# Kernel tuning notes

Hardware: AMD Instinct MI355X
Metric: run time of the kernel (lower is better)

The kernel has to match this reference:

```python
import jax, jax.numpy as jnp
import numpy as np

L = 12        # depth
DIM = 768     # model dim
HEADS = 12
DHEAD = 64
INNER = HEADS * DHEAD   # 768
MLP = 3072
P = 16        # patch size
IMG = 384
C = 3
B = 16
NCLS = 1000
NPATCH = (IMG // P) ** 2   # 576
N = NPATCH + 1             # 577 (cls token)
PATCH_DIM = C * P * P      # 768
SCALE = DIM ** (-0.5)      # NOTE: original scales by dim, not dim_head


def setup_inputs() -> dict:
    key = jax.random.key(0)
    ks = jax.random.split(key, 21)
    rn = lambda k, shape, s=0.02: jax.random.normal(k, shape, dtype=jnp.float32) * s
    return {
        "img": jax.random.normal(ks[0], (B, C, IMG, IMG), dtype=jnp.float32),
        "patch_w": rn(ks[1], (PATCH_DIM, DIM)),
        "patch_b": rn(ks[2], (DIM,)),
        "pos_emb": rn(ks[3], (1, N, DIM), 1.0),
        "cls_tok": rn(ks[4], (1, 1, DIM), 1.0),
        "ln1_w": jnp.ones((L, DIM), jnp.float32),
        "ln1_b": jnp.zeros((L, DIM), jnp.float32),
        "qkv_w": rn(ks[5], (L, DIM, 3 * INNER)),
        "out_w": rn(ks[6], (L, INNER, DIM)),
        "out_b": rn(ks[7], (L, DIM)),
        "ln2_w": jnp.ones((L, DIM), jnp.float32),
        "ln2_b": jnp.zeros((L, DIM), jnp.float32),
        "ff1_w": rn(ks[8], (L, DIM, MLP)),
        "ff1_b": rn(ks[9], (L, MLP)),
        "ff2_w": rn(ks[10], (L, MLP, DIM)),
        "ff2_b": rn(ks[11], (L, DIM)),
        "head_ln_w": jnp.ones((DIM,), jnp.float32),
        "head_ln_b": jnp.zeros((DIM,), jnp.float32),
        "head_w": rn(ks[12], (DIM, NCLS)),
        "head_b": rn(ks[13], (NCLS,)),
    }


def layer_norm(x, w, b, eps=1e-5):
    mu = jnp.mean(x, axis=-1, keepdims=True)
    var = jnp.mean(jnp.square(x - mu), axis=-1, keepdims=True)
    return (x - mu) * jax.lax.rsqrt(var + eps) * w + b


def _vit_forward(img, patch_w, patch_b, pos_emb, cls_tok,
                 ln1_w, ln1_b, qkv_w, out_w, out_b,
                 ln2_w, ln2_b, ff1_w, ff1_b, ff2_w, ff2_b,
                 head_ln_w, head_ln_b, head_w, head_b):
    b = img.shape[0]
    g = IMG // P
    # rearrange 'b c (h p1) (w p2) -> b (h w) (p1 p2 c)'
    x = img.reshape(b, C, g, P, g, P).transpose(0, 2, 4, 3, 5, 1).reshape(b, NPATCH, PATCH_DIM)
    x = x @ patch_w + patch_b                           # [b, 576, dim]
    cls = jnp.broadcast_to(cls_tok, (b, 1, DIM))
    x = jnp.concatenate([cls, x], axis=1) + pos_emb[:, :N]   # [b, 577, dim]

    def block(x, p):
        l1w, l1b, qkvw, ow, ob, l2w, l2b, f1w, f1b, f2w, f2b = p
        # attention (pre-norm, residual inside Attention.forward)
        h = layer_norm(x, l1w, l1b)
        qkv = h @ qkvw                                  # [b, n, 3*inner]
        q, k, v = jnp.split(qkv, 3, axis=-1)
        to_heads = lambda t: t.reshape(b, N, HEADS, DHEAD).transpose(0, 2, 1, 3)
        q, k, v = to_heads(q), to_heads(k), to_heads(v)  # [b, h, n, d]
        dots = jnp.einsum('bhid,bhjd->bhij', q, k) * SCALE
        attn = jax.nn.softmax(dots, axis=-1)
        o = jnp.einsum('bhij,bhjd->bhid', attn, v)
        o = o.transpose(0, 2, 1, 3).reshape(b, N, INNER)
        x = x + (o @ ow + ob)
        # feedforward (pre-norm, residual)
        h2 = layer_norm(x, l2w, l2b)
        h2 = jax.nn.gelu(h2 @ f1w + f1b, approximate=False)
        x = x + (h2 @ f2w + f2b)
        return x, None

    x, _ = jax.lax.scan(block, x,
                        (ln1_w, ln1_b, qkv_w, out_w, out_b,
                         ln2_w, ln2_b, ff1_w, ff1_b, ff2_w, ff2_b))
    cls_out = x[:, 0]                                   # [b, dim]
    return layer_norm(cls_out, head_ln_w, head_ln_b) @ head_w + head_b


def reference(img, patch_w, patch_b, pos_emb, cls_tok,
              ln1_w, ln1_b, qkv_w, out_w, out_b,
              ln2_w, ln2_b, ff1_w, ff1_b, ff2_w, ff2_b,
              head_ln_w, head_ln_b, head_w, head_b):
    return _vit_forward(img, patch_w, patch_b, pos_emb, cls_tok,
                        ln1_w, ln1_b, qkv_w, out_w, out_b,
                        ln2_w, ln2_b, ff1_w, ff1_b, ff2_w, ff2_b,
                        head_ln_w, head_ln_b, head_w, head_b)
```

## Files before the change

### kernel.cpp

```cpp
#include <hip/hip_runtime.h>
#include <cstdint>


typedef __attribute__((ext_vector_type(8))) short bf16x8;
typedef __attribute__((ext_vector_type(4))) float f32x4;

#define NTOK 577

__device__ __forceinline__ ushort f2bf(float f) {
  union { float f; unsigned int u; } x; x.f = f;
  unsigned int r = x.u + 0x7fffu + ((x.u >> 16) & 1u);
  return (ushort)(r >> 16);
}

__device__ __forceinline__ void gload_lds16(const ushort* g, ushort* l) {
  __builtin_amdgcn_global_load_lds(
      (const __attribute__((address_space(1))) unsigned int*)g,
      (__attribute__((address_space(3))) unsigned int*)l, 16, 0, 0);
}

#define VMCNT4 asm volatile("s_waitcnt vmcnt(4)" ::: "memory")
#define VMCNT2 asm volatile("s_waitcnt vmcnt(2)" ::: "memory")
#define VMCNT0 asm volatile("s_waitcnt vmcnt(0)" ::: "memory")
#define LGKM0  asm volatile("s_waitcnt lgkmcnt(0)" ::: "memory")
#define SCHED0 __builtin_amdgcn_sched_barrier(0)
#define BARRIER __builtin_amdgcn_s_barrier()

__device__ __forceinline__ int gsw(int row) {
  return (row & 7) + 2 * ((row >> 4) & 3);
}

__global__ __launch_bounds__(256) void convt_kernel(const float* __restrict__ W,
                                                    ushort* __restrict__ Wt,
                                                    int K, int N) {
  __shared__ float t[32][33];
  const int kb = blockIdx.x * 32, nb = blockIdx.y * 32;
  const int tx = threadIdx.x & 31, ty = threadIdx.x >> 5;
#pragma unroll
  for (int i = 0; i < 32; i += 8)
    t[ty + i][tx] = W[(size_t)(kb + ty + i) * N + (nb + tx)];
  __syncthreads();
#pragma unroll
  for (int i = 0; i < 32; i += 8)
    Wt[(size_t)(nb + ty + i) * K + (kb + tx)] = f2bf(t[tx][ty + i]);
}

__global__ __launch_bounds__(256) void im2col_kernel(const float* __restrict__ img,
                                                     ushort* __restrict__ Ap) {
  const int idx = blockIdx.x * 256 + threadIdx.x;
  const int j = idx % 768;
  const int m = idx / 768;
  const int c = j % 3;
  const int q = j / 3;
  const int px = q & 15, py = q >> 4;
  const int b = m / 576, p = m % 576;
  const int gy = p / 24, gx = p % 24;
  const float v = img[((size_t)(b * 3 + c) * 384 + (gy * 16 + py)) * 384 + (gx * 16 + px)];
  Ap[idx] = f2bf(v);
}

__global__ void clspos_kernel(const float* __restrict__ cls_tok,
                              const float* __restrict__ pos,
                              float* __restrict__ x) {
  const int i = blockIdx.x * 256 + threadIdx.x;
  const int b = i / 768, d = i % 768;
  x[(size_t)b * NTOK * 768 + d] = cls_tok[d] + pos[d];
}

__global__ __launch_bounds__(64) void ln_kernel(const float* __restrict__ x,
                                                const float* __restrict__ w,
                                                const float* __restrict__ bb,
                                                ushort* __restrict__ out) {
  const int row = blockIdx.x, lane = threadIdx.x;
  const float4* xr = reinterpret_cast<const float4*>(x + (size_t)row * 768);
  const float4 v0 = xr[lane], v1 = xr[lane + 64], v2 = xr[lane + 128];
  float vals[12] = {v0.x, v0.y, v0.z, v0.w, v1.x, v1.y, v1.z, v1.w,
                    v2.x, v2.y, v2.z, v2.w};
  float s = 0.f;
#pragma unroll
  for (int i = 0; i < 12; ++i) s += vals[i];
#pragma unroll
  for (int o = 32; o; o >>= 1) s += __shfl_xor(s, o);
  const float mu = s * (1.0f / 768.0f);
  float q = 0.f;
#pragma unroll
  for (int i = 0; i < 12; ++i) { const float d = vals[i] - mu; q += d * d; }
#pragma unroll
  for (int o = 32; o; o >>= 1) q += __shfl_xor(q, o);
  const float rstd = rsqrtf(q * (1.0f / 768.0f) + 1e-5f);
  const float4* w4 = reinterpret_cast<const float4*>(w);
  const float4* b4 = reinterpret_cast<const float4*>(bb);
  ushort* orow = out + (size_t)row * 768;
#pragma unroll
  for (int ch = 0; ch < 3; ++ch) {
    const float4 wv = w4[lane + ch * 64];
    const float4 bv = b4[lane + ch * 64];
    ushort4 u;
    u.x = f2bf((vals[ch * 4 + 0] - mu) * rstd * wv.x + bv.x);
    u.y = f2bf((vals[ch * 4 + 1] - mu) * rstd * wv.y + bv.y);
    u.z = f2bf((vals[ch * 4 + 2] - mu) * rstd * wv.z + bv.z);
    u.w = f2bf((vals[ch * 4 + 3] - mu) * rstd * wv.w + bv.w);
    *reinterpret_cast<ushort4*>(orow + ch * 256 + lane * 4) = u;
  }
}

constexpr int EPI_BF16 = 0;
constexpr int EPI_GELU_BF16 = 1;
constexpr int EPI_RES_F32 = 2;
constexpr int EPI_PATCH = 3;

template <int EPI>
__global__ __launch_bounds__(512, 2) void gemm8_kernel(
    const ushort* __restrict__ A, const ushort* __restrict__ Bt,
    const float* __restrict__ bias, void* __restrict__ Cptr,
    int M, int N, int K, int mt) {
  __shared__ ushort lds[2][2][16384];

  const int nwg = gridDim.x;
  const int orig = blockIdx.x;
  const int q8 = nwg >> 3, r8 = nwg & 7, xcd = orig & 7, sidx = orig >> 3;
  const int wg = (xcd < r8 ? xcd * (q8 + 1) : r8 * (q8 + 1) + (xcd - r8) * q8) + sidx;
  const int tileM = (wg % mt) * 256;
  const int tileN = (wg / mt) * 256;

  const int tid = threadIdx.x;
  const int wave = tid >> 6, lane = tid & 63;
  const int wm = wave >> 2, wn = wave & 3;
  const int lr = lane & 15, lg = lane >> 4;

  f32x4 acc[8][4];
#pragma unroll
  for (int i = 0; i < 8; ++i)
#pragma unroll
    for (int j = 0; j < 4; ++j) acc[i][j] = (f32x4){0.f, 0.f, 0.f, 0.f};

  int rsA[2][2], rsB[2][2];
  const ushort* pA[2][2];
  const ushort* pB[2][2];
#pragma unroll
  for (int h = 0; h < 2; ++h)
#pragma unroll
    for (int g = 0; g < 2; ++g) {
      const int c = wave * 2 + g;
      {
        const int rowst = h * 64 + ((c >> 3) << 7) + ((c & 7) << 3);
        rsA[h][g] = rowst;
        const int row = rowst + (lane >> 3);
        const int lgr = ((lane & 7) - gsw(row)) & 7;
        pA[h][g] = A + (size_t)(tileM + row) * K + lgr * 8;
      }
      {
        const int rowst = h * 32 + ((c >> 2) << 6) + ((c & 3) << 3);
        rsB[h][g] = rowst;
        const int row = rowst + (lane >> 3);
        const int lgr = ((lane & 7) - gsw(row)) & 7;
        pB[h][g] = Bt + (size_t)(tileN + row) * K + lgr * 8;
      }
    }

#define STAGE_A(h, buf, k1)                                   \
  gload_lds16(pA[h][0] + (k1), &lds[buf][0][rsA[h][0] * 64]); \
  gload_lds16(pA[h][1] + (k1), &lds[buf][0][rsA[h][1] * 64]);
#define STAGE_B(h, buf, k1)                                   \
  gload_lds16(pB[h][0] + (k1), &lds[buf][1][rsB[h][0] * 64]); \
  gload_lds16(pB[h][1] + (k1), &lds[buf][1][rsB[h][1] * 64]);

  bf16x8 areg[8], breg[4];
#define LDA8(h, buf)                                                          \
  {                                                                           \
    const ushort* base = &lds[buf][0][0];                                     \
    _Pragma("unroll") for (int mf = 0; mf < 4; ++mf) {                        \
      const int row = wm * 128 + (h) * 64 + mf * 16 + lr;                     \
      _Pragma("unroll") for (int ks = 0; ks < 2; ++ks) {                      \
        const int pg = (ks * 4 + lg + (lr & 7) + 2 * mf) & 7;                 \
        areg[mf * 2 + ks] =                                                   \
            *reinterpret_cast<const bf16x8*>(&base[row * 64 + pg * 8]);       \
      }                                                                       \
    }                                                                         \
  }
#define LDB4(q, buf)                                                          \
  {                                                                           \
    const ushort* base = &lds[buf][1][0];                                     \
    _Pragma("unroll") for (int nf = 0; nf < 2; ++nf) {                        \
      const int row = wn * 64 + (q) * 32 + nf * 16 + lr;                      \
      _Pragma("unroll") for (int ks = 0; ks < 2; ++ks) {                      \
        const int pg = (ks * 4 + lg + (lr & 7) + 2 * (((q)*2 + nf) & 3)) & 7; \
        breg[nf * 2 + ks] =                                                   \
            *reinterpret_cast<const bf16x8*>(&base[row * 64 + pg * 8]);       \
      }                                                                       \
    }                                                                         \
  }
#define MFMA16(h, q)                                                        \
  __builtin_amdgcn_s_setprio(1);                                            \
  _Pragma("unroll") for (int mf = 0; mf < 4; ++mf)                          \
      _Pragma("unroll") for (int nf = 0; nf < 2; ++nf)                      \
          _Pragma("unroll") for (int ks = 0; ks < 2; ++ks)                  \
              acc[(h)*4 + mf][(q)*2 + nf] =                                 \
                  __builtin_amdgcn_mfma_f32_16x16x32_bf16(                  \
                      areg[mf * 2 + ks], breg[nf * 2 + ks],                 \
                      acc[(h)*4 + mf][(q)*2 + nf], 0, 0, 0);                \
  __builtin_amdgcn_s_setprio(0);

  STAGE_A(0, 0, 0);
  STAGE_B(0, 0, 0);
  STAGE_A(1, 0, 0);
  STAGE_B(1, 0, 0);

  const int NT = K >> 6;
  for (int t = 0; t < NT - 1; ++t) {
    const int cb = t & 1, nb = (t + 1) & 1;
    const int k1 = (t + 1) * 64;
    VMCNT4; SCHED0;
    BARRIER;
    LDA8(0, cb);
    LDB4(0, cb);
    STAGE_A(0, nb, k1);
    LGKM0; SCHED0;
    MFMA16(0, 0);
    VMCNT4; SCHED0;
    BARRIER;
    LDA8(1, cb);
    STAGE_B(0, nb, k1);
    LGKM0; SCHED0;
    MFMA16(1, 0);
    VMCNT4; SCHED0;
    BARRIER;
    LDB4(1, cb);
    STAGE_A(1, nb, k1);
    LGKM0; SCHED0;
    MFMA16(1, 1);
    BARRIER;
    LDA8(0, cb);
    STAGE_B(1, nb, k1);
    LGKM0; SCHED0;
    MFMA16(0, 1);
  }

  {
    const int cb = (NT - 1) & 1;
    VMCNT4; SCHED0;
    BARRIER;
    LDA8(0, cb);
    LDB4(0, cb);
    LGKM0; SCHED0;
    MFMA16(0, 0);
    VMCNT2; SCHED0;
    BARRIER;
    LDA8(1, cb);
    LGKM0; SCHED0;
    MFMA16(1, 0);
    VMCNT0; SCHED0;
    BARRIER;
    LDB4(1, cb);
    LGKM0; SCHED0;
    MFMA16(1, 1);
    BARRIER;
    LDA8(0, cb);
    LGKM0; SCHED0;
    MFMA16(0, 1);
  }

#pragma unroll
  for (int am = 0; am < 8; ++am) {
#pragma unroll
    for (int r = 0; r < 4; ++r) {
      const int row = tileM + wm * 128 + (am >> 2) * 64 + (am & 3) * 16 + lg * 4 + r;
      if (row >= M) continue;
#pragma unroll
      for (int an = 0; an < 4; ++an) {
        const int col = tileN + wn * 64 + (an >> 1) * 32 + (an & 1) * 16 + lr;
        float v = acc[am][an][r];
        if constexpr (EPI == EPI_BF16) {
          reinterpret_cast<ushort*>(Cptr)[(size_t)row * N + col] = f2bf(v);
        } else {
          v += bias[col];
          v = 0.5f * v * (1.0f + erff(v * 0.70710678118654752440f));
          reinterpret_cast<ushort*>(Cptr)[(size_t)row * N + col] = f2bf(v);
        }
      }
    }
  }
#undef STAGE_A
#undef STAGE_B
#undef LDA8
#undef LDB4
#undef MFMA16
}

template <int EPI>
__global__ __launch_bounds__(256) void gemm_kernel(
    const ushort* __restrict__ A, const ushort* __restrict__ Bt,
    const float* __restrict__ bias, const float* __restrict__ extra,
    void* __restrict__ Cptr, int M, int N, int K) {
  __shared__ ushort Alds[128 * 32];
  __shared__ ushort Blds[128 * 32];
  const int tid = threadIdx.x;
  const int tileM = blockIdx.x * 128, tileN = blockIdx.y * 128;
  const int wave = tid >> 6, lane = tid & 63;
  const int wrow = (wave >> 1) * 64, wcol = (wave & 1) * 64;
  const int lr = lane & 15, lk = (lane >> 4) * 8;

  f32x4 acc[4][4];
#pragma unroll
  for (int m = 0; m < 4; ++m)
#pragma unroll
    for (int n = 0; n < 4; ++n) acc[m][n] = (f32x4){0.f, 0.f, 0.f, 0.f};

  const int srow = wave * 32 + (lane >> 2);
  const int scol = (lane & 3) * 8;
  const ushort* Ap = A + (size_t)(tileM + srow) * K + scol;
  const ushort* Bp = Bt + (size_t)(tileN + srow) * K + scol;
  ushort* Al0 = &Alds[(wave * 2 + 0) * 512];
  ushort* Al1 = &Alds[(wave * 2 + 1) * 512];
  ushort* Bl0 = &Blds[(wave * 2 + 0) * 512];
  ushort* Bl1 = &Blds[(wave * 2 + 1) * 512];
  const size_t cstride = (size_t)16 * K;

  for (int k0 = 0; k0 < K; k0 += 32) {
    __syncthreads();
    gload_lds16(Ap + k0, Al0);
    gload_lds16(Ap + k0 + cstride, Al1);
    gload_lds16(Bp + k0, Bl0);
    gload_lds16(Bp + k0 + cstride, Bl1);
    __syncthreads();

    bf16x8 af[4], bfr[4];
#pragma unroll
    for (int m = 0; m < 4; ++m)
      af[m] = *reinterpret_cast<const bf16x8*>(&Alds[(wrow + m * 16 + lr) * 32 + lk]);
#pragma unroll
    for (int n = 0; n < 4; ++n)
      bfr[n] = *reinterpret_cast<const bf16x8*>(&Blds[(wcol + n * 16 + lr) * 32 + lk]);
#pragma unroll
    for (int m = 0; m < 4; ++m)
#pragma unroll
      for (int n = 0; n < 4; ++n)
        acc[m][n] = __builtin_amdgcn_mfma_f32_16x16x32_bf16(af[m], bfr[n],
                                                            acc[m][n], 0, 0, 0);
  }

  const int lr4 = (lane >> 4) * 4;
#pragma unroll
  for (int m = 0; m < 4; ++m) {
#pragma unroll
    for (int r = 0; r < 4; ++r) {
      const int row = tileM + wrow + m * 16 + lr4 + r;
      if (row >= M) continue;
#pragma unroll
      for (int n = 0; n < 4; ++n) {
        const int col = tileN + wcol + n * 16 + lr;
        float v = acc[m][n][r];
        if constexpr (EPI == EPI_BF16) {
          reinterpret_cast<ushort*>(Cptr)[(size_t)row * N + col] = f2bf(v);
        } else if constexpr (EPI == EPI_GELU_BF16) {
          v += bias[col];
          v = 0.5f * v * (1.0f + erff(v * 0.70710678118654752440f));
          reinterpret_cast<ushort*>(Cptr)[(size_t)row * N + col] = f2bf(v);
        } else if constexpr (EPI == EPI_RES_F32) {
          v += bias[col] + extra[(size_t)row * N + col];
          reinterpret_cast<float*>(Cptr)[(size_t)row * N + col] = v;
        } else {
          const int bb = row / 576;
          const int p = row - bb * 576;
          v += bias[col] + extra[(size_t)(p + 1) * 768 + col];
          reinterpret_cast<float*>(Cptr)[(size_t)(row + bb + 1) * 768 + col] = v;
        }
      }
    }
  }
}

__global__ __launch_bounds__(256) void attn_kernel(const ushort* __restrict__ qkv,
                                                   ushort* __restrict__ o) {
  __shared__ ushort sK[64 * 64];
  __shared__ ushort sVt[64 * 64];
  __shared__ ushort sP[4][16 * 72];
  const int bh = blockIdx.x;
  const int b = bh / 12, hh = bh % 12;
  const int q0 = blockIdx.y * 64;
  const int tid = threadIdx.x;
  const int wave = tid >> 6, lane = tid & 63;
  const int lr = lane & 15;
  const int lg = lane >> 4;
  const ushort* base = qkv + (size_t)b * NTOK * 2304 + hh * 64;
  const float SC = 0.03608439182435161f;

  bf16x8 qf[2];
  {
    const int qrow = q0 + wave * 16 + lr;
    if (qrow < NTOK) {
      const ushort* qp = base + (size_t)qrow * 2304 + lg * 8;
      qf[0] = *reinterpret_cast<const bf16x8*>(qp);
      qf[1] = *reinterpret_cast<const bf16x8*>(qp + 32);
    } else {
      qf[0] = (bf16x8){0, 0, 0, 0, 0, 0, 0, 0};
      qf[1] = qf[0];
    }
  }

  float mst[4], lst[4];
  f32x4 oacc[4];
#pragma unroll
  for (int i = 0; i < 4; ++i) {
    mst[i] = -1e30f; lst[i] = 0.f;
    oacc[i] = (f32x4){0.f, 0.f, 0.f, 0.f};
  }

  const int skey = tid >> 2;
  const int sc4 = tid & 3;
  const int gswk = gsw(skey);

  for (int t0 = 0; t0 < NTOK; t0 += 64) {
    __syncthreads();
    {
      const int gk = t0 + skey;
      int4 k0v, k1v, v0v, v1v;
      if (gk < NTOK) {
        const int4* kp = reinterpret_cast<const int4*>(base + (size_t)gk * 2304 + 768 + sc4 * 16);
        k0v = kp[0]; k1v = kp[1];
        const int4* vp = reinterpret_cast<const int4*>(base + (size_t)gk * 2304 + 1536 + sc4 * 16);
        v0v = vp[0]; v1v = vp[1];
      } else {
        int4 z; z.x = z.y = z.z = z.w = 0;
        k0v = k1v = v0v = v1v = z;
      }
      *reinterpret_cast<int4*>(&sK[skey * 64 + (((2 * sc4 + 0) + gswk) & 7) * 8]) = k0v;
      *reinterpret_cast<int4*>(&sK[skey * 64 + (((2 * sc4 + 1) + gswk) & 7) * 8]) = k1v;
      const ushort* vs = reinterpret_cast<const ushort*>(&v0v);
      const ushort* vs2 = reinterpret_cast<const ushort*>(&v1v);
#pragma unroll
      for (int i = 0; i < 8; ++i) {
        const int d0 = sc4 * 16 + i;
        const int pg0 = ((skey >> 3) + gsw(d0)) & 7;
        sVt[d0 * 64 + pg0 * 8 + (skey & 7)] = vs[i];
        const int d1 = sc4 * 16 + 8 + i;
        const int pg1 = ((skey >> 3) + gsw(d1)) & 7;
        sVt[d1 * 64 + pg1 * 8 + (skey & 7)] = vs2[i];
      }
    }
    __syncthreads();

    f32x4 sacc[4];
#pragma unroll
    for (int n = 0; n < 4; ++n) sacc[n] = (f32x4){0.f, 0.f, 0.f, 0.f};
#pragma unroll
    for (int n = 0; n < 4; ++n) {
      const int row = n * 16 + lr;
      const int rot = (lr & 7) + 2 * n;
      const bf16x8 kf0 = *reinterpret_cast<const bf16x8*>(&sK[row * 64 + ((lg + rot) & 7) * 8]);
      const bf16x8 kf1 = *reinterpret_cast<const bf16x8*>(&sK[row * 64 + ((4 + lg + rot) & 7) * 8]);
      sacc[n] = __builtin_amdgcn_mfma_f32_16x16x32_bf16(qf[0], kf0, sacc[n], 0, 0, 0);
      sacc[n] = __builtin_amdgcn_mfma_f32_16x16x32_bf16(qf[1], kf1, sacc[n], 0, 0, 0);
    }

    float s[4][4], pm[4];
#pragma unroll
    for (int reg = 0; reg < 4; ++reg) pm[reg] = -1e30f;
#pragma unroll
    for (int n = 0; n < 4; ++n)
#pragma unroll
      for (int reg = 0; reg < 4; ++reg) {
        float v = sacc[n][reg] * SC;
        if (t0 + n * 16 + lr >= NTOK) v = -1e30f;
        s[n][reg] = v;
        pm[reg] = fmaxf(pm[reg], v);
      }
#pragma unroll
    for (int off = 1; off < 16; off <<= 1)
#pragma unroll
      for (int reg = 0; reg < 4; ++reg) pm[reg] = fmaxf(pm[reg], __shfl_xor(pm[reg], off));

    float al[4], rs[4];
#pragma unroll
    for (int reg = 0; reg < 4; ++reg) {
      const float mn = fmaxf(mst[reg], pm[reg]);
      al[reg] = __expf(mst[reg] - mn);
      mst[reg] = mn;
      rs[reg] = 0.f;
    }
#pragma unroll
    for (int n = 0; n < 4; ++n)
#pragma unroll
      for (int reg = 0; reg < 4; ++reg) {
        s[n][reg] = __expf(s[n][reg] - mst[reg]);
        rs[reg] += s[n][reg];
      }
#pragma unroll
    for (int off = 1; off < 16; off <<= 1)
#pragma unroll
      for (int reg = 0; reg < 4; ++reg) rs[reg] += __shfl_xor(rs[reg], off);
#pragma unroll
    for (int reg = 0; reg < 4; ++reg) {
      lst[reg] = lst[reg] * al[reg] + rs[reg];
#pragma unroll
      for (int n = 0; n < 4; ++n) oacc[n][reg] *= al[reg];
    }

#pragma unroll
    for (int n = 0; n < 4; ++n)
#pragma unroll
      for (int reg = 0; reg < 4; ++reg)
        sP[wave][(lg * 4 + reg) * 72 + n * 16 + lr] = f2bf(s[n][reg]);

    const bf16x8 pf0 = *reinterpret_cast<const bf16x8*>(&sP[wave][lr * 72 + lg * 8]);
    const bf16x8 pf1 = *reinterpret_cast<const bf16x8*>(&sP[wave][lr * 72 + 32 + lg * 8]);
#pragma unroll
    for (int n = 0; n < 4; ++n) {
      const int row = n * 16 + lr;
      const int rot = (lr & 7) + 2 * n;
      const bf16x8 vf0 = *reinterpret_cast<const bf16x8*>(&sVt[row * 64 + ((lg + rot) & 7) * 8]);
      const bf16x8 vf1 = *reinterpret_cast<const bf16x8*>(&sVt[row * 64 + ((4 + lg + rot) & 7) * 8]);
      oacc[n] = __builtin_amdgcn_mfma_f32_16x16x32_bf16(pf0, vf0, oacc[n], 0, 0, 0);
      oacc[n] = __builtin_amdgcn_mfma_f32_16x16x32_bf16(pf1, vf1, oacc[n], 0, 0, 0);
    }
  }

#pragma unroll
  for (int reg = 0; reg < 4; ++reg) {
    const int q = q0 + wave * 16 + lg * 4 + reg;
    if (q >= NTOK) continue;
    const float inv = 1.0f / lst[reg];
    ushort* op = o + (size_t)(b * NTOK + q) * 768 + hh * 64;
#pragma unroll
    for (int n = 0; n < 4; ++n) op[n * 16 + lr] = f2bf(oacc[n][reg] * inv);
  }
}

__global__ __launch_bounds__(256) void head_kernel(const float* __restrict__ x,
                                                   const float* __restrict__ lw,
                                                   const float* __restrict__ lb,
                                                   const float* __restrict__ hw,
                                                   const float* __restrict__ hb,
                                                   float* __restrict__ out) {
  __shared__ float srow[768];
  __shared__ float sred[8];
  const int b = blockIdx.x, tid = threadIdx.x;
  const float* xr = x + (size_t)b * NTOK * 768;
  for (int i = tid; i < 768; i += 256) srow[i] = xr[i];
  __syncthreads();
  float part = srow[tid] + srow[tid + 256] + srow[tid + 512];
#pragma unroll
  for (int off = 32; off; off >>= 1) part += __shfl_xor(part, off);
  if ((tid & 63) == 0) sred[tid >> 6] = part;
  __syncthreads();
  const float mu = (sred[0] + sred[1] + sred[2] + sred[3]) * (1.0f / 768.0f);
  const float d0 = srow[tid] - mu, d1 = srow[tid + 256] - mu, d2 = srow[tid + 512] - mu;
  float vp = d0 * d0 + d1 * d1 + d2 * d2;
#pragma unroll
  for (int off = 32; off; off >>= 1) vp += __shfl_xor(vp, off);
  if ((tid & 63) == 0) sred[4 + (tid >> 6)] = vp;
  __syncthreads();
  const float rstd = rsqrtf((sred[4] + sred[5] + sred[6] + sred[7]) * (1.0f / 768.0f) + 1e-5f);
  for (int i = tid; i < 768; i += 256) srow[i] = (srow[i] - mu) * rstd * lw[i] + lb[i];
  __syncthreads();
  const int c = blockIdx.y * 250 + tid;
  if (tid < 250 && c < 1000) {
    float a = 0.f;
#pragma unroll 4
    for (int k = 0; k < 768; ++k) a += srow[k] * hw[(size_t)k * 1000 + c];
    out[b * 1000 + c] = a + hb[c];
  }
}

extern "C" void kernel_launch(void* const* d_in, const int* in_sizes, int n_in,
                              void* d_out, int out_size, void* d_ws, size_t ws_size,
                              hipStream_t stream) {
  const float* img     = (const float*)d_in[0];
  const float* patch_w = (const float*)d_in[1];
  const float* patch_b = (const float*)d_in[2];
  const float* pos_emb = (const float*)d_in[3];
  const float* cls_tok = (const float*)d_in[4];
  const float* ln1_w   = (const float*)d_in[5];
  const float* ln1_b   = (const float*)d_in[6];
  const float* qkv_w   = (const float*)d_in[7];
  const float* out_w   = (const float*)d_in[8];
  const float* out_b   = (const float*)d_in[9];
  const float* ln2_w   = (const float*)d_in[10];
  const float* ln2_b   = (const float*)d_in[11];
  const float* ff1_w   = (const float*)d_in[12];
  const float* ff1_b   = (const float*)d_in[13];
  const float* ff2_w   = (const float*)d_in[14];
  const float* ff2_b   = (const float*)d_in[15];
  const float* hln_w   = (const float*)d_in[16];
  const float* hln_b   = (const float*)d_in[17];
  const float* head_w  = (const float*)d_in[18];
  const float* head_b  = (const float*)d_in[19];
  float* outp = (float*)d_out;

  char* wsp = (char*)d_ws;
  auto alloc = [&](size_t bytes) {
    char* p = wsp;
    wsp += (bytes + 255) & ~(size_t)255;
    return p;
  };
  float*  x    = (float*) alloc((size_t)9232 * 768 * 4);
  ushort* h    = (ushort*)alloc((size_t)9232 * 768 * 2);
  ushort* qkvb = (ushort*)alloc((size_t)9232 * 2304 * 2);
  ushort* mlp  = (ushort*)alloc((size_t)9232 * 3072 * 2);
  ushort* wq   = (ushort*)alloc((size_t)768 * 2304 * 2);
  ushort* wo   = (ushort*)alloc((size_t)768 * 768 * 2);
  ushort* w1   = (ushort*)alloc((size_t)768 * 3072 * 2);
  ushort* w2   = (ushort*)alloc((size_t)3072 * 768 * 2);
  ushort* apatch = mlp;
  ushort* wpatch = wq;

  convt_kernel<<<dim3(24, 24), 256, 0, stream>>>(patch_w, wpatch, 768, 768);
  im2col_kernel<<<27648, 256, 0, stream>>>(img, apatch);
  gemm_kernel<EPI_PATCH><<<dim3(72, 6), 256, 0, stream>>>(
      apatch, wpatch, patch_b, pos_emb, x, 9216, 768, 768);
  clspos_kernel<<<48, 256, 0, stream>>>(cls_tok, pos_emb, x);

  for (int l = 0; l < 12; ++l) {
    ln_kernel<<<9232, 64, 0, stream>>>(x, ln1_w + l * 768, ln1_b + l * 768, h);
    convt_kernel<<<dim3(24, 72), 256, 0, stream>>>(qkv_w + (size_t)l * 768 * 2304, wq, 768, 2304);
    gemm8_kernel<EPI_BF16><<<37 * 9, 512, 0, stream>>>(
        h, wq, nullptr, qkvb, 9232, 2304, 768, 37);
    attn_kernel<<<dim3(192, 10), 256, 0, stream>>>(qkvb, h);
    convt_kernel<<<dim3(24, 24), 256, 0, stream>>>(out_w + (size_t)l * 768 * 768, wo, 768, 768);
    gemm_kernel<EPI_RES_F32><<<dim3(73, 6), 256, 0, stream>>>(
        h, wo, out_b + l * 768, x, x, 9232, 768, 768);
    ln_kernel<<<9232, 64, 0, stream>>>(x, ln2_w + l * 768, ln2_b + l * 768, h);
    convt_kernel<<<dim3(24, 96), 256, 0, stream>>>(ff1_w + (size_t)l * 768 * 3072, w1, 768, 3072);
    gemm8_kernel<EPI_GELU_BF16><<<37 * 12, 512, 0, stream>>>(
        h, w1, ff1_b + l * 3072, mlp, 9232, 3072, 768, 37);
    convt_kernel<<<dim3(96, 24), 256, 0, stream>>>(ff2_w + (size_t)l * 3072 * 768, w2, 3072, 768);
    gemm_kernel<EPI_RES_F32><<<dim3(73, 6), 256, 0, stream>>>(
        mlp, w2, ff2_b + l * 768, x, x, 9232, 768, 3072);
  }

  head_kernel<<<dim3(16, 4), 256, 0, stream>>>(x, hln_w, hln_b, head_w, head_b, outp);
}
```

Before: 4.638 ms.

## Double-buffer swizzled 128x128 GEMM with BK=64 and XCD-aware tile remap

Replaces the single-buffer BK=32 128x128 GEMM used for the patch, out-projection and FF2 projections with a double-buffered BK=64 kernel. Global-to-LDS loads for the next K tile are issued before the current tile is computed. LDS rows are XOR-swizzled to avoid bank conflicts, MFMA sections get raised priority, and workgroups are remapped across the 8 XCDs for L2 locality. The cost is twice the LDS per block (64KB), which may lower occupancy.

```diff
diff --git a/kernel.cpp b/kernel.cpp
--- a/kernel.cpp
+++ b/kernel.cpp
@@ -288,17 +288,24 @@
 }
 
 template <int EPI>
-__global__ __launch_bounds__(256) void gemm_kernel(
+__global__ __launch_bounds__(256) void gemmP_kernel(
     const ushort* __restrict__ A, const ushort* __restrict__ Bt,
     const float* __restrict__ bias, const float* __restrict__ extra,
-    void* __restrict__ Cptr, int M, int N, int K) {
-  __shared__ ushort Alds[128 * 32];
-  __shared__ ushort Blds[128 * 32];
+    void* __restrict__ Cptr, int M, int N, int K, int mt) {
+  __shared__ ushort ldsA[2][128 * 64];
+  __shared__ ushort ldsB[2][128 * 64];
+
+  const int nwg = gridDim.x;
+  const int orig = blockIdx.x;
+  const int q8 = nwg >> 3, r8 = nwg & 7, xcd = orig & 7, sidx = orig >> 3;
+  const int wg = (xcd < r8 ? xcd * (q8 + 1) : r8 * (q8 + 1) + (xcd - r8) * q8) + sidx;
+  const int tileM = (wg % mt) * 128;
+  const int tileN = (wg / mt) * 128;
+
   const int tid = threadIdx.x;
-  const int tileM = blockIdx.x * 128, tileN = blockIdx.y * 128;
   const int wave = tid >> 6, lane = tid & 63;
-  const int wrow = (wave >> 1) * 64, wcol = (wave & 1) * 64;
-  const int lr = lane & 15, lk = (lane >> 4) * 8;
+  const int wm = wave >> 1, wn = wave & 1;
+  const int lr = lane & 15, lg = lane >> 4;
 
   f32x4 acc[4][4];
 #pragma unroll
@@ -306,50 +313,77 @@
 #pragma unroll
     for (int n = 0; n < 4; ++n) acc[m][n] = (f32x4){0.f, 0.f, 0.f, 0.f};
 
-  const int srow = wave * 32 + (lane >> 2);
-  const int scol = (lane & 3) * 8;
-  const ushort* Ap = A + (size_t)(tileM + srow) * K + scol;
-  const ushort* Bp = Bt + (size_t)(tileN + srow) * K + scol;
-  ushort* Al0 = &Alds[(wave * 2 + 0) * 512];
-  ushort* Al1 = &Alds[(wave * 2 + 1) * 512];
-  ushort* Bl0 = &Blds[(wave * 2 + 0) * 512];
-  ushort* Bl1 = &Blds[(wave * 2 + 1) * 512];
-  const size_t cstride = (size_t)16 * K;
-
-  for (int k0 = 0; k0 < K; k0 += 32) {
-    __syncthreads();
-    gload_lds16(Ap + k0, Al0);
-    gload_lds16(Ap + k0 + cstride, Al1);
-    gload_lds16(Bp + k0, Bl0);
-    gload_lds16(Bp + k0 + cstride, Bl1);
-    __syncthreads();
-
-    bf16x8 af[4], bfr[4];
-#pragma unroll
-    for (int m = 0; m < 4; ++m)
-      af[m] = *reinterpret_cast<const bf16x8*>(&Alds[(wrow + m * 16 + lr) * 32 + lk]);
-#pragma unroll
-    for (int n = 0; n < 4; ++n)
-      bfr[n] = *reinterpret_cast<const bf16x8*>(&Blds[(wcol + n * 16 + lr) * 32 + lk]);
-#pragma unroll
-    for (int m = 0; m < 4; ++m)
-#pragma unroll
-      for (int n = 0; n < 4; ++n)
-        acc[m][n] = __builtin_amdgcn_mfma_f32_16x16x32_bf16(af[m], bfr[n],
-                                                            acc[m][n], 0, 0, 0);
-  }
-
-  const int lr4 = (lane >> 4) * 4;
-#pragma unroll
-  for (int m = 0; m < 4; ++m) {
+  const ushort* pA[4];
+  const ushort* pB[4];
+  int dst[4];
+#pragma unroll
+  for (int i = 0; i < 4; ++i) {
+    const int c = wave * 4 + i;
+    const int rowst = c * 8;
+    dst[i] = rowst * 64;
+    const int row = rowst + (lane >> 3);
+    const int lgr = ((lane & 7) - gsw(row)) & 7;
+    pA[i] = A + (size_t)(tileM + row) * K + lgr * 8;
+    pB[i] = Bt + (size_t)(tileN + row) * K + lgr * 8;
+  }
+
+#define PSTAGE(buf, kk)                              \
+  _Pragma("unroll") for (int i = 0; i < 4; ++i)      \
+      gload_lds16(pA[i] + (kk), &ldsA[buf][dst[i]]); \
+  _Pragma("unroll") for (int i = 0; i < 4; ++i)      \
+      gload_lds16(pB[i] + (kk), &ldsB[buf][dst[i]]);
+
+  PSTAGE(0, 0);
+
+  const int NT = K >> 6;
+  int cb = 0;
+  for (int t = 0; t < NT; ++t) {
+    VMCNT0; SCHED0;
+    BARRIER;
+    if (t + 1 < NT) { PSTAGE(cb ^ 1, (t + 1) * 64); }
+    bf16x8 a[8], b[8];
+#pragma unroll
+    for (int mf = 0; mf < 4; ++mf) {
+      const int row = wm * 64 + mf * 16 + lr;
+#pragma unroll
+      for (int ks = 0; ks < 2; ++ks) {
+        const int pg = (ks * 4 + lg + (lr & 7) + 2 * mf) & 7;
+        a[mf * 2 + ks] = *reinterpret_cast<const bf16x8*>(&ldsA[cb][row * 64 + pg * 8]);
+      }
+    }
+#pragma unroll
+    for (int nf = 0; nf < 4; ++nf) {
+      const int row = wn * 64 + nf * 16 + lr;
+#pragma unroll
+      for (int ks = 0; ks < 2; ++ks) {
+        const int pg = (ks * 4 + lg + (lr & 7) + 2 * nf) & 7;
+        b[nf * 2 + ks] = *reinterpret_cast<const bf16x8*>(&ldsB[cb][row * 64 + pg * 8]);
+      }
+    }
+    LGKM0; SCHED0;
+    __builtin_amdgcn_s_setprio(1);
+#pragma unroll
+    for (int mf = 0; mf < 4; ++mf)
+#pragma unroll
+      for (int nf = 0; nf < 4; ++nf)
+#pragma unroll
+        for (int ks = 0; ks < 2; ++ks)
+          acc[mf][nf] = __builtin_amdgcn_mfma_f32_16x16x32_bf16(
+              a[mf * 2 + ks], b[nf * 2 + ks], acc[mf][nf], 0, 0, 0);
+    __builtin_amdgcn_s_setprio(0);
+    cb ^= 1;
+  }
+
+#pragma unroll
+  for (int mf = 0; mf < 4; ++mf) {
 #pragma unroll
     for (int r = 0; r < 4; ++r) {
-      const int row = tileM + wrow + m * 16 + lr4 + r;
+      const int row = tileM + wm * 64 + mf * 16 + lg * 4 + r;
       if (row >= M) continue;
 #pragma unroll
-      for (int n = 0; n < 4; ++n) {
-        const int col = tileN + wcol + n * 16 + lr;
-        float v = acc[m][n][r];
+      for (int nf = 0; nf < 4; ++nf) {
+        const int col = tileN + wn * 64 + nf * 16 + lr;
+        float v = acc[mf][nf][r];
         if constexpr (EPI == EPI_BF16) {
           reinterpret_cast<ushort*>(Cptr)[(size_t)row * N + col] = f2bf(v);
         } else if constexpr (EPI == EPI_GELU_BF16) {
@@ -368,6 +402,7 @@
       }
     }
   }
+#undef PSTAGE
 }
 
 __global__ __launch_bounds__(256) void attn_kernel(const ushort* __restrict__ qkv,
@@ -606,8 +641,8 @@
 
   convt_kernel<<<dim3(24, 24), 256, 0, stream>>>(patch_w, wpatch, 768, 768);
   im2col_kernel<<<27648, 256, 0, stream>>>(img, apatch);
-  gemm_kernel<EPI_PATCH><<<dim3(72, 6), 256, 0, stream>>>(
-      apatch, wpatch, patch_b, pos_emb, x, 9216, 768, 768);
+  gemmP_kernel<EPI_PATCH><<<72 * 6, 256, 0, stream>>>(
+      apatch, wpatch, patch_b, pos_emb, x, 9216, 768, 768, 72);
   clspos_kernel<<<48, 256, 0, stream>>>(cls_tok, pos_emb, x);
 
   for (int l = 0; l < 12; ++l) {
@@ -617,15 +652,15 @@
         h, wq, nullptr, qkvb, 9232, 2304, 768, 37);
     attn_kernel<<<dim3(192, 10), 256, 0, stream>>>(qkvb, h);
     convt_kernel<<<dim3(24, 24), 256, 0, stream>>>(out_w + (size_t)l * 768 * 768, wo, 768, 768);
-    gemm_kernel<EPI_RES_F32><<<dim3(73, 6), 256, 0, stream>>>(
-        h, wo, out_b + l * 768, x, x, 9232, 768, 768);
+    gemmP_kernel<EPI_RES_F32><<<73 * 6, 256, 0, stream>>>(
+        h, wo, out_b + l * 768, x, x, 9232, 768, 768, 73);
     ln_kernel<<<9232, 64, 0, stream>>>(x, ln2_w + l * 768, ln2_b + l * 768, h);
     convt_kernel<<<dim3(24, 96), 256, 0, stream>>>(ff1_w + (size_t)l * 768 * 3072, w1, 768, 3072);
     gemm8_kernel<EPI_GELU_BF16><<<37 * 12, 512, 0, stream>>>(
         h, w1, ff1_b + l * 3072, mlp, 9232, 3072, 768, 37);
     convt_kernel<<<dim3(96, 24), 256, 0, stream>>>(ff2_w + (size_t)l * 3072 * 768, w2, 3072, 768);
-    gemm_kernel<EPI_RES_F32><<<dim3(73, 6), 256, 0, stream>>>(
-        mlp, w2, ff2_b + l * 768, x, x, 9232, 768, 3072);
+    gemmP_kernel<EPI_RES_F32><<<73 * 6, 256, 0, stream>>>(
+        mlp, w2, ff2_b + l * 768, x, x, 9232, 768, 3072, 73);
   }
 
   head_kernel<<<dim3(16, 4), 256, 0, stream>>>(x, hln_w, hln_b, head_w, head_b, outp);
```

Result: faster. 4.280 ms (-7.7%).
